# Kernel optimization log

Measured on AMD Instinct MI355X. Metric: run time of the kernel, lower is better.

The kernel has to match this reference:

```python
import jax, jax.numpy as jnp
import numpy as np

D_MODEL = 2048
NUM_HEADS = 16
NUM_KV_HEADS = 4
HEAD_DIM = D_MODEL // NUM_HEADS          # 128
GROUPS = NUM_HEADS // NUM_KV_HEADS       # 4
ROT_DIM = HEAD_DIM // 2                  # 64
QK_EPS = 1e-6
B, L = 2, 2048


def setup_inputs() -> dict:
    key = jax.random.key(0)
    kx, kq, kk, kv, ko = jax.random.split(key, 5)
    x = jax.random.normal(kx, (B, L, D_MODEL), dtype=jnp.float32)
    # realistic RoPE tables, broadcastable against [B, L, H, ROT_DIM]
    inv_freq = 1.0 / (10000.0 ** (np.arange(ROT_DIM, dtype=np.float32) / ROT_DIM))
    ang = np.arange(L, dtype=np.float32)[:, None] * inv_freq[None, :]   # [L, ROT_DIM]
    cos = jnp.asarray(np.cos(ang), dtype=jnp.float32)[None, :, None, :]
    sin = jnp.asarray(np.sin(ang), dtype=jnp.float32)[None, :, None, :]
    s = 1.0 / np.sqrt(D_MODEL)
    Wq = jax.random.normal(kq, (D_MODEL, D_MODEL), dtype=jnp.float32) * s
    Wk = jax.random.normal(kk, (D_MODEL, NUM_KV_HEADS * HEAD_DIM), dtype=jnp.float32) * s
    Wv = jax.random.normal(kv, (D_MODEL, NUM_KV_HEADS * HEAD_DIM), dtype=jnp.float32) * s
    Wo = jax.random.normal(ko, (D_MODEL, D_MODEL), dtype=jnp.float32) * s
    return {"x": x, "cos": cos, "sin": sin, "Wq": Wq, "Wk": Wk, "Wv": Wv, "Wo": Wo}


def _apply_rope(t, cos, sin):
    # t: [B, L, H, HEAD_DIM]; half-split rotation as in the original
    x1, x2 = t[..., :ROT_DIM], t[..., ROT_DIM:]
    return jnp.concatenate([x1 * cos - x2 * sin, x2 * cos + x1 * sin], axis=-1)


def _rms_norm(t):
    ms = jnp.mean(jnp.square(t), axis=-1, keepdims=True)
    return t * jax.lax.rsqrt(ms + QK_EPS)


def reference(x, cos, sin, Wq, Wk, Wv, Wo):
    b, l, _ = x.shape
    q = (x @ Wq).reshape(b, l, NUM_HEADS, HEAD_DIM)
    k = (x @ Wk).reshape(b, l, NUM_KV_HEADS, HEAD_DIM)
    v = (x @ Wv).reshape(b, l, NUM_KV_HEADS, HEAD_DIM)
    q = _apply_rope(q, cos, sin)
    k = _apply_rope(k, cos, sin)
    # qk_norm=True: RMS-normalize q and k over head_dim
    q = _rms_norm(q)
    k = _rms_norm(k)
    # GQA: repeat kv heads to match q heads (matches reshape/tile/reshape)
    k = jnp.repeat(k, GROUPS, axis=2)   # [b, l, NUM_HEADS, HEAD_DIM]
    v = jnp.repeat(v, GROUPS, axis=2)
    scores = jnp.einsum('blhd,bmhd->bhlm', q, k) / np.float32(np.sqrt(HEAD_DIM))
    causal = jnp.tril(jnp.ones((l, l), dtype=bool))[None, None, :, :]
    scores = jnp.where(causal, scores, jnp.float32(-1e9))
    attn = jax.nn.softmax(scores, axis=-1)            # [b, h, l(q), m(kv)]
    out = jnp.einsum('bhlm,bmhd->blhd', attn, v).reshape(b, l, D_MODEL)
    return out @ Wo
```

## Files before the change

kernel.cpp:

```cpp
#include <hip/hip_runtime.h>
#include <stdint.h>

#define D_MODEL 2048
#define L_SEQ   2048
#define BATCH   2
#define NH      16
#define NKV     4
#define HD      128
#define ROT     64
#define M_ROWS  (BATCH * L_SEQ)
#define N_QKV   (D_MODEL + 2 * NKV * HD)

typedef short bf16x8 __attribute__((ext_vector_type(8)));
typedef float f32x4  __attribute__((ext_vector_type(4)));
typedef float f32x16 __attribute__((ext_vector_type(16)));

__device__ __forceinline__ unsigned short f2b(float f) {
  union { float f; unsigned u; } v; v.f = f;
  unsigned r = v.u + 0x7FFFu + ((v.u >> 16) & 1u);
  return (unsigned short)(r >> 16);
}

__device__ __forceinline__ unsigned cvtpk_bf16(float a, float b) {
  unsigned r;
  asm("v_cvt_pk_bf16_f32 %0, %1, %2" : "=v"(r) : "v"(a), "v"(b));
  return r;
}

__global__ void cvt_bf16_kernel(const float* __restrict__ in,
                                unsigned short* __restrict__ out, int n4) {
  int i = blockIdx.x * blockDim.x + threadIdx.x;
  if (i < n4) {
    float4 v = ((const float4*)in)[i];
    ushort4 o;
    o.x = f2b(v.x); o.y = f2b(v.y); o.z = f2b(v.z); o.w = f2b(v.w);
    ((ushort4*)out)[i] = o;
  }
}

__global__ void build_wqkv_t(const float* __restrict__ Wq, const float* __restrict__ Wk,
                             const float* __restrict__ Wv, unsigned short* __restrict__ Wt) {
  __shared__ float tile[32][33];
  int k0 = blockIdx.x * 32;
  int n0 = blockIdx.y * 32;
  const float* W; int c0, ldw;
  if (n0 < D_MODEL)            { W = Wq; c0 = n0;                 ldw = D_MODEL; }
  else if (n0 < D_MODEL + 512) { W = Wk; c0 = n0 - D_MODEL;       ldw = 512; }
  else                         { W = Wv; c0 = n0 - D_MODEL - 512; ldw = 512; }
  int tx = threadIdx.x, ty = threadIdx.y;
#pragma unroll
  for (int i = 0; i < 32; i += 8)
    tile[ty + i][tx] = W[(size_t)(k0 + ty + i) * ldw + c0 + tx];
  __syncthreads();
#pragma unroll
  for (int i = 0; i < 32; i += 8)
    Wt[(size_t)(n0 + ty + i) * D_MODEL + k0 + tx] = f2b(tile[tx][ty + i]);
}

__global__ void build_wo_t(const float* __restrict__ Wo, unsigned short* __restrict__ Wt) {
  __shared__ float tile[32][33];
  int k0 = blockIdx.x * 32;
  int n0 = blockIdx.y * 32;
  int tx = threadIdx.x, ty = threadIdx.y;
#pragma unroll
  for (int i = 0; i < 32; i += 8)
    tile[ty + i][tx] = Wo[(size_t)(k0 + ty + i) * D_MODEL + n0 + tx];
  __syncthreads();
#pragma unroll
  for (int i = 0; i < 32; i += 8)
    Wt[(size_t)(n0 + ty + i) * D_MODEL + k0 + tx] = f2b(tile[tx][ty + i]);
}

#define BM 128
#define BN 128
#define BKg 64

__device__ __forceinline__ void async16(void* lds, const void* g) {
  __builtin_amdgcn_global_load_lds((const __attribute__((address_space(1))) void*)g,
                                   (__attribute__((address_space(3))) void*)lds, 16, 0, 0);
}

__global__ __launch_bounds__(256, 2)
void gemm_bt(const unsigned short* __restrict__ A, const unsigned short* __restrict__ Bt,
             float* __restrict__ C, int M, int N, int K) {
  __shared__ unsigned short As[BM * BKg];
  __shared__ unsigned short Bs[BN * BKg];
  int m0 = blockIdx.y * BM;
  int n0 = blockIdx.x * BN;
  int tid = threadIdx.x;
  int lane = tid & 63;
  int wave = __builtin_amdgcn_readfirstlane(tid >> 6);
  int wr = wave >> 1, wc = wave & 1;
  int lgrp = lane >> 4, lidx = lane & 15;

  f32x4 acc[4][4];
#pragma unroll
  for (int i = 0; i < 4; i++)
#pragma unroll
    for (int j = 0; j < 4; j++) { acc[i][j][0]=0.f; acc[i][j][1]=0.f; acc[i][j][2]=0.f; acc[i][j][3]=0.f; }

  for (int k0 = 0; k0 < K; k0 += BKg) {
#pragma unroll
    for (int iss = 0; iss < 4; iss++) {
      int idx = iss * 256 + tid;
      int row = idx >> 3, cch = idx & 7;
      int lbase = (iss * 256 + wave * 64) * 8;
      async16((void*)(As + lbase), A  + (size_t)(m0 + row) * K + k0 + cch * 8);
      async16((void*)(Bs + lbase), Bt + (size_t)(n0 + row) * K + k0 + cch * 8);
    }
    __syncthreads();
#pragma unroll
    for (int kk = 0; kk < BKg; kk += 32) {
      bf16x8 af[4], bfr[4];
#pragma unroll
      for (int i = 0; i < 4; i++) {
        af[i]  = *(const bf16x8*)(As + (wr * 64 + i * 16 + lidx) * BKg + kk + lgrp * 8);
        bfr[i] = *(const bf16x8*)(Bs + (wc * 64 + i * 16 + lidx) * BKg + kk + lgrp * 8);
      }
#pragma unroll
      for (int i = 0; i < 4; i++)
#pragma unroll
        for (int j = 0; j < 4; j++)
          acc[i][j] = __builtin_amdgcn_mfma_f32_16x16x32_bf16(af[i], bfr[j], acc[i][j], 0, 0, 0);
    }
    __syncthreads();
  }
#pragma unroll
  for (int i = 0; i < 4; i++) {
    int rowb = m0 + wr * 64 + i * 16 + lgrp * 4;
#pragma unroll
    for (int j = 0; j < 4; j++) {
      int col = n0 + wc * 64 + j * 16 + lidx;
#pragma unroll
      for (int r = 0; r < 4; r++)
        C[(size_t)(rowb + r) * N + col] = acc[i][j][r];
    }
  }
}

__global__ __launch_bounds__(256)
void rope_rms_kernel(const float* __restrict__ QKV, const float* __restrict__ cosp,
                     const float* __restrict__ sinp, unsigned short* __restrict__ Qb,
                     unsigned short* __restrict__ Kb) {
  int row = blockIdx.x;
  int b = row >> 11, l = row & 2047;
  int lane = threadIdx.x & 63;
  int wave = threadIdx.x >> 6;
  const float* src = QKV + (size_t)row * N_QKV;
  float c = cosp[l * ROT + lane];
  float s = sinp[l * ROT + lane];
  for (int hh = wave; hh < NH + NKV; hh += 4) {
    bool isq = hh < NH;
    int col0 = isq ? hh * HD : D_MODEL + (hh - NH) * HD;
    float x1 = src[col0 + lane];
    float x2 = src[col0 + 64 + lane];
    float o1 = x1 * c - x2 * s;
    float o2 = x2 * c + x1 * s;
    float ss = o1 * o1 + o2 * o2;
#pragma unroll
    for (int mk = 1; mk < 64; mk <<= 1) ss += __shfl_xor(ss, mk, 64);
    float rn = rsqrtf(ss * (1.f / 128.f) + 1e-6f);
    if (isq) rn *= 0.08838834764831845f;
    o1 *= rn; o2 *= rn;
    unsigned short* dst = isq ? (Qb + ((size_t)(b * NH + hh) * L_SEQ + l) * HD)
                              : (Kb + ((size_t)(b * NKV + (hh - NH)) * L_SEQ + l) * HD);
    dst[lane]      = f2b(o1);
    dst[lane + 64] = f2b(o2);
  }
}

__global__ void vt_build(const float* __restrict__ QKV, unsigned short* __restrict__ Vt) {
  __shared__ float tile[32][33];
  int z = blockIdx.z;
  int l0 = blockIdx.x * 32;
  int d0 = blockIdx.y * 32;
  int b = z >> 2, kh = z & 3;
  int tx = threadIdx.x, ty = threadIdx.y;
  int colbase = D_MODEL + NKV * HD + kh * HD + d0;
#pragma unroll
  for (int i = 0; i < 32; i += 8)
    tile[ty + i][tx] = QKV[(size_t)(b * L_SEQ + l0 + ty + i) * N_QKV + colbase + tx];
  __syncthreads();
#pragma unroll
  for (int i = 0; i < 32; i += 8)
    Vt[((size_t)z * HD + d0 + ty + i) * L_SEQ + l0 + tx] = f2b(tile[tx][ty + i]);
}

#define KSTRIDE 256
#define VSTRIDE 64
#define TILEB   16384

__global__ __launch_bounds__(256, 2)
void attn128_kernel(const unsigned short* __restrict__ Qb, const unsigned short* __restrict__ Kb,
                    const unsigned short* __restrict__ Vt, unsigned short* __restrict__ AttO) {
  __shared__ char lds[2 * TILEB];
  int blk = blockIdx.x;
  int qt = 15 - (blk >> 5);
  int bh = blk & 31;
  int b = bh >> 4, h = bh & 15, kh = h >> 2;
  int tid = threadIdx.x;
  int lane = tid & 63;
  int wave = __builtin_amdgcn_readfirstlane(tid >> 6);
  int col = lane & 31;
  int hi  = lane >> 5;
  int q0 = qt * 128 + wave * 32;

  const unsigned short* Q   = Qb + ((size_t)(b * NH + h) * L_SEQ + q0) * HD;
  const unsigned short* Kg  = Kb + (size_t)(b * NKV + kh) * L_SEQ * HD;
  const unsigned short* Vtg = Vt + (size_t)(b * NKV + kh) * HD * L_SEQ;

  bf16x8 qf[8];
#pragma unroll
  for (int c = 0; c < 8; c++)
    qf[c] = *(const bf16x8*)(Q + (size_t)col * HD + c * 16 + hi * 8);

  f32x16 o[4];
#pragma unroll
  for (int d0 = 0; d0 < 4; d0++)
#pragma unroll
    for (int r = 0; r < 16; r++) o[d0][r] = 0.f;
  float m = -1e30f, lsum = 0.f;

  int NT = 4 * (qt + 1);
  int tmax = 4 * qt + wave;

  auto STAGE = [&](char* base, int t) {
    int kv0 = t * 32;
    char* ldsK = base;
    char* ldsV = base + 8192;
    int wb = wave * 64;
#pragma unroll
    for (int r = 0; r < 2; r++) {
      int slot = r * 256 + tid;
      int row = slot >> 4, s16 = slot & 15;
      const char* src = (const char*)Kg + (size_t)(kv0 + row) * KSTRIDE + ((s16 ^ (row & 7)) << 4);
      async16(ldsK + (size_t)(r * 256 + wb) * 16, src);
    }
#pragma unroll
    for (int r = 0; r < 2; r++) {
      int slot = r * 256 + tid;
      int row = slot >> 2, s4 = slot & 3;
      const char* src = (const char*)Vtg + (size_t)row * (L_SEQ * 2) + (size_t)kv0 * 2 + ((s4 ^ (row & 3)) << 4);
      async16(ldsV + (size_t)(r * 256 + wb) * 16, src);
    }
  };

  STAGE(lds, 0);
  __syncthreads();

  int cur = 0;
  for (int t = 0; t < NT; t++) {
    if (t + 1 < NT) STAGE(lds + (cur ^ 1) * TILEB, t + 1);

    if (t <= tmax) {
      const char* KB = lds + cur * TILEB;
      const char* VB = KB + 8192;
      int kv0 = t * 32;
      f32x16 sA, sB;
#pragma unroll
      for (int r = 0; r < 16; r++) { sA[r] = 0.f; sB[r] = 0.f; }
#pragma unroll
      for (int c = 0; c < 4; c++) {
        bf16x8 kf = *(const bf16x8*)(KB + col * KSTRIDE + ((32 * c + 16 * hi) ^ ((col & 7) << 4)));
        sA = __builtin_amdgcn_mfma_f32_32x32x16_bf16(kf, qf[c], sA, 0, 0, 0);
      }
#pragma unroll
      for (int c = 4; c < 8; c++) {
        bf16x8 kf = *(const bf16x8*)(KB + col * KSTRIDE + ((32 * c + 16 * hi) ^ ((col & 7) << 4)));
        sB = __builtin_amdgcn_mfma_f32_32x32x16_bf16(kf, qf[c], sB, 0, 0, 0);
      }
      f32x16 s = sA + sB;
      if (t == tmax) {
#pragma unroll
        for (int r = 0; r < 16; r++) {
          int kvl = (r & 3) + 8 * (r >> 2) + 4 * hi;
          if (kvl > col) s[r] = -1e30f;
        }
      }
      float mx = s[0];
#pragma unroll
      for (int r = 1; r < 16; r++) mx = fmaxf(mx, s[r]);
      mx = fmaxf(mx, __shfl_xor(mx, 32, 64));
      if (!__all(mx <= m + 8.f)) {
        float mnew = fmaxf(m, mx);
        float sf = __expf(m - mnew);
        lsum *= sf;
#pragma unroll
        for (int d0 = 0; d0 < 4; d0++)
#pragma unroll
          for (int r = 0; r < 16; r++) o[d0][r] *= sf;
        m = mnew;
      }
      float ps = 0.f;
#pragma unroll
      for (int r = 0; r < 16; r++) { s[r] = __expf(s[r] - m); ps += s[r]; }
      lsum += ps + __shfl_xor(ps, 32, 64);
#pragma unroll
      for (int w2 = 0; w2 < 2; w2++) {
        unsigned c01 = cvtpk_bf16(s[w2*8+0], s[w2*8+1]);
        unsigned c23 = cvtpk_bf16(s[w2*8+2], s[w2*8+3]);
        unsigned c45 = cvtpk_bf16(s[w2*8+4], s[w2*8+5]);
        unsigned c67 = cvtpk_bf16(s[w2*8+6], s[w2*8+7]);
        unsigned x01 = (unsigned)__shfl_xor((int)c01, 32, 64);
        unsigned x23 = (unsigned)__shfl_xor((int)c23, 32, 64);
        unsigned x45 = (unsigned)__shfl_xor((int)c45, 32, 64);
        unsigned x67 = (unsigned)__shfl_xor((int)c67, 32, 64);
        union { unsigned u[4]; bf16x8 v; } pb;
        pb.u[0] = hi ? x45 : c01;
        pb.u[1] = hi ? x67 : c23;
        pb.u[2] = hi ? c45 : x01;
        pb.u[3] = hi ? c67 : x23;
#pragma unroll
        for (int d0 = 0; d0 < 4; d0++) {
          bf16x8 vf = *(const bf16x8*)(VB + (d0 * 32 + col) * VSTRIDE + ((32 * w2 + 16 * hi) ^ ((col & 3) << 4)));
          o[d0] = __builtin_amdgcn_mfma_f32_32x32x16_bf16(vf, pb.v, o[d0], 0, 0, 0);
        }
      }
    }
    __syncthreads();
    cur ^= 1;
  }

  float* tr = (float*)(lds + wave * 4352);
  float inv = 1.f / lsum;
  unsigned short* orow = AttO + (size_t)(b * L_SEQ + q0 + col) * D_MODEL + h * HD;
#pragma unroll
  for (int d0 = 0; d0 < 4; d0++) {
#pragma unroll
    for (int r = 0; r < 16; r++)
      tr[((r & 3) + 8 * (r >> 2) + 4 * hi) * 33 + col] = o[d0][r] * inv;
    __syncthreads();
    union { unsigned u[8]; } pk;
#pragma unroll
    for (int t = 0; t < 8; t++) {
      float a  = tr[(hi * 16 + 2 * t) * 33 + col];
      float bb = tr[(hi * 16 + 2 * t + 1) * 33 + col];
      pk.u[t] = ((unsigned)f2b(a)) | (((unsigned)f2b(bb)) << 16);
    }
    *(uint4*)(orow + d0 * 32 + hi * 16)     = *(uint4*)&pk.u[0];
    *(uint4*)(orow + d0 * 32 + hi * 16 + 8) = *(uint4*)&pk.u[4];
    __syncthreads();
  }
}

extern "C" void kernel_launch(void* const* d_in, const int* in_sizes, int n_in,
                              void* d_out, int out_size, void* d_ws, size_t ws_size,
                              hipStream_t stream) {
  const float* x    = (const float*)d_in[0];
  const float* cosp = (const float*)d_in[1];
  const float* sinp = (const float*)d_in[2];
  const float* Wq   = (const float*)d_in[3];
  const float* Wk   = (const float*)d_in[4];
  const float* Wv   = (const float*)d_in[5];
  const float* Wo   = (const float*)d_in[6];
  float* out = (float*)d_out;

  char* ws = (char*)d_ws;
  unsigned short* Xb   = (unsigned short*)ws; ws += (size_t)M_ROWS * D_MODEL * 2;
  unsigned short* Wt   = (unsigned short*)ws; ws += (size_t)N_QKV * D_MODEL * 2;
  unsigned short* Wot  = (unsigned short*)ws; ws += (size_t)D_MODEL * D_MODEL * 2;
  float*          QKV  = (float*)ws;          ws += (size_t)M_ROWS * N_QKV * 4;
  unsigned short* Qb   = (unsigned short*)ws; ws += (size_t)BATCH * NH * L_SEQ * HD * 2;
  unsigned short* Kb   = (unsigned short*)ws; ws += (size_t)BATCH * NKV * L_SEQ * HD * 2;
  unsigned short* Vt   = (unsigned short*)ws; ws += (size_t)BATCH * NKV * HD * L_SEQ * 2;
  unsigned short* AttO = (unsigned short*)ws; ws += (size_t)M_ROWS * D_MODEL * 2;

  cvt_bf16_kernel<<<(M_ROWS * D_MODEL / 4 + 255) / 256, 256, 0, stream>>>(x, Xb, M_ROWS * D_MODEL / 4);
  build_wqkv_t<<<dim3(64, 96), dim3(32, 8), 0, stream>>>(Wq, Wk, Wv, Wt);
  build_wo_t<<<dim3(64, 64), dim3(32, 8), 0, stream>>>(Wo, Wot);
  gemm_bt<<<dim3(N_QKV / BN, M_ROWS / BM), 256, 0, stream>>>(Xb, Wt, QKV, M_ROWS, N_QKV, D_MODEL);
  rope_rms_kernel<<<M_ROWS, 256, 0, stream>>>(QKV, cosp, sinp, Qb, Kb);
  vt_build<<<dim3(64, 4, 8), dim3(32, 8), 0, stream>>>(QKV, Vt);
  attn128_kernel<<<dim3(512), 256, 0, stream>>>(Qb, Kb, Vt, AttO);
  gemm_bt<<<dim3(D_MODEL / BN, M_ROWS / BM), 256, 0, stream>>>(AttO, Wot, out, M_ROWS, D_MODEL, D_MODEL);
}
```

Baseline: 338.5 us.

## Store QKV projection in bf16 and shrink attention query tiles to 64

The QKV GEMM now writes its output as bf16 instead of fp32, so the rope/rms and V-transpose kernels read half as many bytes and vt_build no longer converts. Attention is changed from 128-query blocks of 4 waves to 64-query blocks of 2 waves, with a 1024-block grid and an XOR-based query-tile order that spreads causal work across blocks. This reduces intermediate memory traffic and aims for better load balance and occupancy. The cost is extra rounding of pre-norm Q/K/V, and each K/V tile is now loaded by fewer waves, so there is less reuse per load.

```diff
diff --git a/kernel.cpp b/kernel.cpp
--- a/kernel.cpp
+++ b/kernel.cpp
@@ -19,6 +19,10 @@
   union { float f; unsigned u; } v; v.f = f;
   unsigned r = v.u + 0x7FFFu + ((v.u >> 16) & 1u);
   return (unsigned short)(r >> 16);
+}
+
+__device__ __forceinline__ float b2f(unsigned short u) {
+  union { unsigned u; float f; } v; v.u = ((unsigned)u) << 16; return v.f;
 }
 
 __device__ __forceinline__ unsigned cvtpk_bf16(float a, float b) {
@@ -80,9 +84,10 @@
                                    (__attribute__((address_space(3))) void*)lds, 16, 0, 0);
 }
 
+template<bool BF16OUT>
 __global__ __launch_bounds__(256, 2)
 void gemm_bt(const unsigned short* __restrict__ A, const unsigned short* __restrict__ Bt,
-             float* __restrict__ C, int M, int N, int K) {
+             void* __restrict__ Cv, int M, int N, int K) {
   __shared__ unsigned short As[BM * BKg];
   __shared__ unsigned short Bs[BN * BKg];
   int m0 = blockIdx.y * BM;
@@ -132,28 +137,32 @@
     for (int j = 0; j < 4; j++) {
       int col = n0 + wc * 64 + j * 16 + lidx;
 #pragma unroll
-      for (int r = 0; r < 4; r++)
-        C[(size_t)(rowb + r) * N + col] = acc[i][j][r];
+      for (int r = 0; r < 4; r++) {
+        if constexpr (BF16OUT)
+          ((unsigned short*)Cv)[(size_t)(rowb + r) * N + col] = f2b(acc[i][j][r]);
+        else
+          ((float*)Cv)[(size_t)(rowb + r) * N + col] = acc[i][j][r];
+      }
     }
   }
 }
 
 __global__ __launch_bounds__(256)
-void rope_rms_kernel(const float* __restrict__ QKV, const float* __restrict__ cosp,
+void rope_rms_kernel(const unsigned short* __restrict__ QKV, const float* __restrict__ cosp,
                      const float* __restrict__ sinp, unsigned short* __restrict__ Qb,
                      unsigned short* __restrict__ Kb) {
   int row = blockIdx.x;
   int b = row >> 11, l = row & 2047;
   int lane = threadIdx.x & 63;
   int wave = threadIdx.x >> 6;
-  const float* src = QKV + (size_t)row * N_QKV;
+  const unsigned short* src = QKV + (size_t)row * N_QKV;
   float c = cosp[l * ROT + lane];
   float s = sinp[l * ROT + lane];
   for (int hh = wave; hh < NH + NKV; hh += 4) {
     bool isq = hh < NH;
     int col0 = isq ? hh * HD : D_MODEL + (hh - NH) * HD;
-    float x1 = src[col0 + lane];
-    float x2 = src[col0 + 64 + lane];
+    float x1 = b2f(src[col0 + lane]);
+    float x2 = b2f(src[col0 + 64 + lane]);
     float o1 = x1 * c - x2 * s;
     float o2 = x2 * c + x1 * s;
     float ss = o1 * o1 + o2 * o2;
@@ -169,8 +178,8 @@
   }
 }
 
-__global__ void vt_build(const float* __restrict__ QKV, unsigned short* __restrict__ Vt) {
-  __shared__ float tile[32][33];
+__global__ void vt_build(const unsigned short* __restrict__ QKV, unsigned short* __restrict__ Vt) {
+  __shared__ unsigned short tile[32][33];
   int z = blockIdx.z;
   int l0 = blockIdx.x * 32;
   int d0 = blockIdx.y * 32;
@@ -183,27 +192,27 @@
   __syncthreads();
 #pragma unroll
   for (int i = 0; i < 32; i += 8)
-    Vt[((size_t)z * HD + d0 + ty + i) * L_SEQ + l0 + tx] = f2b(tile[tx][ty + i]);
+    Vt[((size_t)z * HD + d0 + ty + i) * L_SEQ + l0 + tx] = tile[tx][ty + i];
 }
 
 #define KSTRIDE 256
 #define VSTRIDE 64
 #define TILEB   16384
 
-__global__ __launch_bounds__(256, 2)
-void attn128_kernel(const unsigned short* __restrict__ Qb, const unsigned short* __restrict__ Kb,
-                    const unsigned short* __restrict__ Vt, unsigned short* __restrict__ AttO) {
+__global__ __launch_bounds__(128, 2)
+void attn64_kernel(const unsigned short* __restrict__ Qb, const unsigned short* __restrict__ Kb,
+                   const unsigned short* __restrict__ Vt, unsigned short* __restrict__ AttO) {
   __shared__ char lds[2 * TILEB];
   int blk = blockIdx.x;
-  int qt = 15 - (blk >> 5);
-  int bh = blk & 31;
+  int bh = blk >> 5;
+  int qt = (blk & 31) ^ bh;
   int b = bh >> 4, h = bh & 15, kh = h >> 2;
   int tid = threadIdx.x;
   int lane = tid & 63;
   int wave = __builtin_amdgcn_readfirstlane(tid >> 6);
   int col = lane & 31;
   int hi  = lane >> 5;
-  int q0 = qt * 128 + wave * 32;
+  int q0 = qt * 64 + wave * 32;
 
   const unsigned short* Q   = Qb + ((size_t)(b * NH + h) * L_SEQ + q0) * HD;
   const unsigned short* Kg  = Kb + (size_t)(b * NKV + kh) * L_SEQ * HD;
@@ -221,8 +230,8 @@
     for (int r = 0; r < 16; r++) o[d0][r] = 0.f;
   float m = -1e30f, lsum = 0.f;
 
-  int NT = 4 * (qt + 1);
-  int tmax = 4 * qt + wave;
+  int NT = 2 * (qt + 1);
+  int tmax = 2 * qt + wave;
 
   auto STAGE = [&](char* base, int t) {
     int kv0 = t * 32;
@@ -230,18 +239,18 @@
     char* ldsV = base + 8192;
     int wb = wave * 64;
 #pragma unroll
-    for (int r = 0; r < 2; r++) {
-      int slot = r * 256 + tid;
+    for (int r = 0; r < 4; r++) {
+      int slot = r * 128 + tid;
       int row = slot >> 4, s16 = slot & 15;
       const char* src = (const char*)Kg + (size_t)(kv0 + row) * KSTRIDE + ((s16 ^ (row & 7)) << 4);
-      async16(ldsK + (size_t)(r * 256 + wb) * 16, src);
-    }
-#pragma unroll
-    for (int r = 0; r < 2; r++) {
-      int slot = r * 256 + tid;
+      async16(ldsK + (size_t)(r * 128 + wb) * 16, src);
+    }
+#pragma unroll
+    for (int r = 0; r < 4; r++) {
+      int slot = r * 128 + tid;
       int row = slot >> 2, s4 = slot & 3;
       const char* src = (const char*)Vtg + (size_t)row * (L_SEQ * 2) + (size_t)kv0 * 2 + ((s4 ^ (row & 3)) << 4);
-      async16(ldsV + (size_t)(r * 256 + wb) * 16, src);
+      async16(ldsV + (size_t)(r * 128 + wb) * 16, src);
     }
   };
 
@@ -255,7 +264,6 @@
     if (t <= tmax) {
       const char* KB = lds + cur * TILEB;
       const char* VB = KB + 8192;
-      int kv0 = t * 32;
       f32x16 sA, sB;
 #pragma unroll
       for (int r = 0; r < 16; r++) { sA[r] = 0.f; sB[r] = 0.f; }
@@ -359,7 +367,7 @@
   unsigned short* Xb   = (unsigned short*)ws; ws += (size_t)M_ROWS * D_MODEL * 2;
   unsigned short* Wt   = (unsigned short*)ws; ws += (size_t)N_QKV * D_MODEL * 2;
   unsigned short* Wot  = (unsigned short*)ws; ws += (size_t)D_MODEL * D_MODEL * 2;
-  float*          QKV  = (float*)ws;          ws += (size_t)M_ROWS * N_QKV * 4;
+  unsigned short* QKVb = (unsigned short*)ws; ws += (size_t)M_ROWS * N_QKV * 4;
   unsigned short* Qb   = (unsigned short*)ws; ws += (size_t)BATCH * NH * L_SEQ * HD * 2;
   unsigned short* Kb   = (unsigned short*)ws; ws += (size_t)BATCH * NKV * L_SEQ * HD * 2;
   unsigned short* Vt   = (unsigned short*)ws; ws += (size_t)BATCH * NKV * HD * L_SEQ * 2;
@@ -368,9 +376,9 @@
   cvt_bf16_kernel<<<(M_ROWS * D_MODEL / 4 + 255) / 256, 256, 0, stream>>>(x, Xb, M_ROWS * D_MODEL / 4);
   build_wqkv_t<<<dim3(64, 96), dim3(32, 8), 0, stream>>>(Wq, Wk, Wv, Wt);
   build_wo_t<<<dim3(64, 64), dim3(32, 8), 0, stream>>>(Wo, Wot);
-  gemm_bt<<<dim3(N_QKV / BN, M_ROWS / BM), 256, 0, stream>>>(Xb, Wt, QKV, M_ROWS, N_QKV, D_MODEL);
-  rope_rms_kernel<<<M_ROWS, 256, 0, stream>>>(QKV, cosp, sinp, Qb, Kb);
-  vt_build<<<dim3(64, 4, 8), dim3(32, 8), 0, stream>>>(QKV, Vt);
-  attn128_kernel<<<dim3(512), 256, 0, stream>>>(Qb, Kb, Vt, AttO);
-  gemm_bt<<<dim3(D_MODEL / BN, M_ROWS / BM), 256, 0, stream>>>(AttO, Wot, out, M_ROWS, D_MODEL, D_MODEL);
-}
+  gemm_bt<true><<<dim3(N_QKV / BN, M_ROWS / BM), 256, 0, stream>>>(Xb, Wt, QKVb, M_ROWS, N_QKV, D_MODEL);
+  rope_rms_kernel<<<M_ROWS, 256, 0, stream>>>(QKVb, cosp, sinp, Qb, Kb);
+  vt_build<<<dim3(64, 4, 8), dim3(32, 8), 0, stream>>>(QKVb, Vt);
+  attn64_kernel<<<dim3(1024), 128, 0, stream>>>(Qb, Kb, Vt, AttO);
+  gemm_bt<false><<<dim3(D_MODEL / BN, M_ROWS / BM), 256, 0, stream>>>(AttO, Wot, out, M_ROWS, D_MODEL, D_MODEL);
+}
```

Result: no change. 337.0 us (-0.4%).
